# Performance work log

Measured on AMD Instinct MI355X. Metric: run time of the kernel, lower is better.

## Reference

```python
import jax, jax.numpy as jnp
import numpy as np
from jax import lax

EPS_GN = 1e-5
EPS_LN = 1e-5
EPS_ADJ = 1e-6


def group_norm(x, g, b, groups=8, eps=EPS_GN):
    # x: (N, C, T); PyTorch GroupNorm: normalize over (C//groups, T) per group
    N, C, T = x.shape
    xr = x.reshape(N, groups, C // groups, T)
    m = xr.mean(axis=(2, 3), keepdims=True)
    v = xr.var(axis=(2, 3), keepdims=True)
    xr = (xr - m) * lax.rsqrt(v + eps)
    return xr.reshape(N, C, T) * g[None, :, None] + b[None, :, None]


def layer_norm(x, g, b, eps=EPS_LN):
    m = x.mean(axis=-1, keepdims=True)
    v = x.var(axis=-1, keepdims=True)
    return (x - m) * lax.rsqrt(v + eps) * g + b


def conv1d(x, w, stride, pad):
    # x: (N, Cin, T), w: (Cout, Cin, K), no bias
    return lax.conv_general_dilated(x, w, window_strides=(stride,), padding=[(pad, pad)],
                                    dimension_numbers=('NCH', 'OIH', 'NCH'))


def setup_inputs() -> dict:
    key = jax.random.key(0)
    ks = jax.random.split(key, 16)
    B, C, T = 256, 4, 4096
    TW, D, N = 64, 128, 4
    x = jax.random.normal(ks[0], (B, C, T), dtype=jnp.float32)
    conv1_w = jax.random.normal(ks[1], (TW, 1, 9), dtype=jnp.float32) * 0.1
    gn1_g = jnp.ones((TW,), jnp.float32)
    gn1_b = jnp.zeros((TW,), jnp.float32)
    conv2_w = jax.random.normal(ks[2], (TW, TW, 7), dtype=jnp.float32) * 0.05
    gn2_g = jnp.ones((TW,), jnp.float32)
    gn2_b = jnp.zeros((TW,), jnp.float32)
    proj_w = jax.random.normal(ks[3], (D, TW), dtype=jnp.float32) * 0.1
    proj_b = jnp.zeros((D,), jnp.float32)
    A = jnp.eye(N, dtype=jnp.float32) + 0.05 * jax.random.normal(ks[4], (N, N), dtype=jnp.float32)
    lin1_w = jax.random.normal(ks[5], (D, D), dtype=jnp.float32) * 0.08
    ln1_g = jnp.ones((D,), jnp.float32)
    ln1_b = jnp.zeros((D,), jnp.float32)
    lin2_w = jax.random.normal(ks[6], (D, D), dtype=jnp.float32) * 0.08
    ln2_g = jnp.ones((D,), jnp.float32)
    ln2_b = jnp.zeros((D,), jnp.float32)
    on_g = jnp.ones((D,), jnp.float32)
    on_b = jnp.zeros((D,), jnp.float32)
    return dict(x=x, conv1_w=conv1_w, gn1_g=gn1_g, gn1_b=gn1_b, conv2_w=conv2_w,
                gn2_g=gn2_g, gn2_b=gn2_b, proj_w=proj_w, proj_b=proj_b, A=A,
                lin1_w=lin1_w, ln1_g=ln1_g, ln1_b=ln1_b, lin2_w=lin2_w,
                ln2_g=ln2_g, ln2_b=ln2_b, on_g=on_g, on_b=on_b)


def reference(x, conv1_w, gn1_g, gn1_b, conv2_w, gn2_g, gn2_b, proj_w, proj_b, A,
              lin1_w, ln1_g, ln1_b, lin2_w, ln2_g, ln2_b, on_g, on_b):
    B, C, T = x.shape
    D = proj_w.shape[0]
    # The per-channel Python loop in the original shares the same temporal net;
    # fold channels into the batch dim and run the convs once.
    h = x.reshape(B * C, 1, T)
    h = jax.nn.gelu(group_norm(conv1d(h, conv1_w, 2, 4), gn1_g, gn1_b), approximate=False)
    h = jax.nn.gelu(group_norm(conv1d(h, conv2_w, 2, 3), gn2_g, gn2_b), approximate=False)
    h = h.mean(axis=-1)                      # (B*C, TW)
    v = h @ proj_w.T + proj_b                # (B*C, D)
    H = v.reshape(B, C, D)                   # node features, N = C channels
    # normalized adjacency: D^{-1/2} (A + I) D^{-1/2}
    A_tilde = A + jnp.eye(A.shape[0], dtype=A.dtype)
    deg = A_tilde.sum(axis=1)
    d_inv_sqrt = (deg + EPS_ADJ) ** -0.5
    A_hat = d_inv_sqrt[:, None] * A_tilde * d_inv_sqrt[None, :]
    for lw, lg, lb in ((lin1_w, ln1_g, ln1_b), (lin2_w, ln2_g, ln2_b)):
        Hm = jnp.einsum('nm,bmd->bnd', A_hat, H)
        H = jax.nn.gelu(layer_norm(Hm @ lw.T, lg, lb), approximate=False)
    H = layer_norm(H, on_g, on_b)
    return H.mean(axis=1)                    # (B, D)
```

## Files before the change

kernel.cpp:

```cpp
#include <hip/hip_runtime.h>
#include <hip/hip_fp16.h>
#include <math.h>

#define NS   1024
#define TIN  4096
#define T1   2048
#define T2   1024
#define TW   64
#define NG   8
#define DD   128

typedef __attribute__((ext_vector_type(8))) _Float16 f16x8;
typedef __attribute__((ext_vector_type(4))) float    f32x4;

__device__ __forceinline__ float gelu_fast(float x) {
  float t = x * x;
  float p = fmaf(0.044715f, t, 1.0f);
  float u = 2.3022038f * x * p;
  float e = exp2f(u);
  float r = __builtin_amdgcn_rcpf(e + 1.0f);
  return fmaf(-x, r, x);
}

__global__ __launch_bounds__(64) void k_stats1(
    const float* __restrict__ x, const float* __restrict__ w1,
    float* __restrict__ stats1) {
  int n = blockIdx.x;
  __shared__ float xw[4112];
  const float* xr = x + (size_t)n * TIN;
  for (int i = threadIdx.x; i < 4112; i += 64) {
    int xi = i - 4;
    xw[i] = (xi >= 0 && xi < TIN) ? xr[xi] : 0.f;
  }
  __syncthreads();
  float C[45], S[9];
#pragma unroll
  for (int c = 0; c < 45; c++) C[c] = 0.f;
#pragma unroll
  for (int i = 0; i < 9; i++) S[i] = 0.f;
  int l = threadIdx.x;
  for (int j = 0; j < 32; j++) {
    int t = l + 64 * j;
    float w[9];
#pragma unroll
    for (int i = 0; i < 9; i++) w[i] = xw[2 * t + i];
#pragma unroll
    for (int i = 0; i < 9; i++) S[i] += w[i];
    int c = 0;
#pragma unroll
    for (int i = 0; i < 9; i++)
#pragma unroll
      for (int jj = i; jj < 9; jj++) { C[c] = fmaf(w[i], w[jj], C[c]); c++; }
  }
#pragma unroll
  for (int off = 1; off < 64; off <<= 1) {
#pragma unroll
    for (int i = 0; i < 9; i++) S[i] += __shfl_xor(S[i], off, 64);
#pragma unroll
    for (int c = 0; c < 45; c++) C[c] += __shfl_xor(C[c], off, 64);
  }
  float wv[9];
#pragma unroll
  for (int i = 0; i < 9; i++) wv[i] = w1[l * 9 + i];
  float sm = 0.f, sq = 0.f;
  {
    int c = 0;
#pragma unroll
    for (int i = 0; i < 9; i++) {
      sm = fmaf(wv[i], S[i], sm);
#pragma unroll
      for (int jj = i; jj < 9; jj++) {
        float f = (jj == i) ? wv[i] * wv[jj] : 2.f * wv[i] * wv[jj];
        sq = fmaf(f, C[c], sq); c++;
      }
    }
  }
#pragma unroll
  for (int off = 1; off < 8; off <<= 1) {
    sm += __shfl_xor(sm, off, 64);
    sq += __shfl_xor(sq, off, 64);
  }
  if ((l & 7) == 0) {
    float m = sm * (1.f / 16384.f);
    float v = sq * (1.f / 16384.f) - m * m;
    stats1[(n * NG + (l >> 3)) * 2 + 0] = m;
    stats1[(n * NG + (l >> 3)) * 2 + 1] = rsqrtf(v + 1e-5f);
  }
}

__global__ __launch_bounds__(256) void k_prep(
    const float* __restrict__ w2, const float* __restrict__ w1,
    _Float16* __restrict__ w2tf, _Float16* __restrict__ w1h) {
  int idx = blockIdx.x * 256 + threadIdx.x;
  if (idx < 7 * 64 * 64) {
    int kk = idx >> 12;
    int r = idx & 4095;
    int co = r >> 6, ci = r & 63;
    w2tf[idx] = (_Float16)w2[(co * 64 + ci) * 7 + kk];
  } else {
    int r = idx - 28672;
    if (r < 64 * 32) {
      int ci = r >> 5, k = r & 31;
      w1h[r] = (k < 9) ? (_Float16)w1[ci * 9 + k] : (_Float16)0.f;
    }
  }
}

__global__ __launch_bounds__(256, 6) void k_conv(
    const float* __restrict__ x, const _Float16* __restrict__ w1h,
    const float* __restrict__ g1, const float* __restrict__ b1,
    const float* __restrict__ stats1, const _Float16* __restrict__ w2tf,
    __half* __restrict__ y2, float* __restrict__ stats2) {
  constexpr int ROWS = 144, HS = 72;
  __shared__ _Float16 h1s[ROWS * HS];
  __shared__ _Float16 xh[320];
  __shared__ float scs[TW], bss[TW];

  const int tid = threadIdx.x;
  const int n = blockIdx.x >> 4;
  const int tile = blockIdx.x & 15;
  const int t0 = tile << 6;
  const bool chk = (tile == 0) || (tile == 15);

  const float* xr = x + (size_t)n * TIN;
  for (int i = tid; i < 320; i += 256) {
    int xi = 4 * t0 - 10 + i;
    xh[i] = (i < 278 && xi >= 0 && xi < TIN) ? (_Float16)xr[xi] : (_Float16)0.f;
  }
  if (tid < TW) {
    int ci = tid, g = ci >> 3;
    float m = stats1[(n * NG + g) * 2 + 0];
    float is = stats1[(n * NG + g) * 2 + 1];
    float s = is * g1[ci];
    scs[ci] = s;
    bss[ci] = b1[ci] - m * s;
  }
  __syncthreads();

  const int lane = tid & 63;
  const int wv = tid >> 6;
  const int m = lane & 15;
  const int q = lane >> 4;

  {
    f16x8 w1f[4];
#pragma unroll
    for (int nt = 0; nt < 4; nt++)
      w1f[nt] = *(const f16x8*)&w1h[(nt * 16 + m) * 32 + 8 * q];
    float sc4[4], bs4[4];
#pragma unroll
    for (int nt = 0; nt < 4; nt++) {
      sc4[nt] = scs[nt * 16 + m];
      bs4[nt] = bss[nt * 16 + m];
    }
    for (int mt = wv; mt < 9; mt += 4) {
      int r0 = mt * 16;
      int xi0 = 2 * (r0 + m) + 8 * q;
      uint4 uu;
      uu.x = *(const unsigned*)&xh[xi0 + 0];
      uu.y = *(const unsigned*)&xh[xi0 + 2];
      uu.z = *(const unsigned*)&xh[xi0 + 4];
      uu.w = *(const unsigned*)&xh[xi0 + 6];
      f16x8 af = __builtin_bit_cast(f16x8, uu);
      int rowb = r0 + 4 * q;
#pragma unroll
      for (int nt = 0; nt < 4; nt++) {
        f32x4 d = __builtin_amdgcn_mfma_f32_16x16x32_f16(
            af, w1f[nt], (f32x4){0.f, 0.f, 0.f, 0.f}, 0, 0, 0);
#pragma unroll
        for (int r = 0; r < 4; r++) {
          float v = gelu_fast(fmaf(d[r], sc4[nt], bs4[nt]));
          if (chk) {
            int tp = 2 * t0 - 3 + rowb + r;
            if ((unsigned)tp >= (unsigned)T1) v = 0.f;
          }
          h1s[(rowb + r) * HS + nt * 16 + m] = (_Float16)v;
        }
      }
    }
  }
  __syncthreads();

  const int co0 = wv * 16 + m;
  f32x4 acc[4];
#pragma unroll
  for (int mt = 0; mt < 4; mt++) acc[mt] = (f32x4){0.f, 0.f, 0.f, 0.f};

  for (int kk = 0; kk < 7; kk++) {
    f16x8 bfr[2];
#pragma unroll
    for (int ks = 0; ks < 2; ks++)
      bfr[ks] = *(const f16x8*)&w2tf[(kk * 64 + co0) * 64 + 32 * ks + 8 * q];
#pragma unroll
    for (int mt = 0; mt < 4; mt++) {
      int tl = 2 * (mt * 16 + m) + kk;
      f16x8 a0 = *(const f16x8*)&h1s[tl * HS + 8 * q];
      f16x8 a1 = *(const f16x8*)&h1s[tl * HS + 32 + 8 * q];
      acc[mt] = __builtin_amdgcn_mfma_f32_16x16x32_f16(a0, bfr[0], acc[mt], 0, 0, 0);
      acc[mt] = __builtin_amdgcn_mfma_f32_16x16x32_f16(a1, bfr[1], acc[mt], 0, 0, 0);
    }
  }

  float sum = 0.f, ssq = 0.f;
#pragma unroll
  for (int mt = 0; mt < 4; mt++)
#pragma unroll
    for (int r = 0; r < 4; r++) {
      float v = acc[mt][r];
      sum += v; ssq += v * v;
    }
  sum += __shfl_xor(sum, 1, 64);  ssq += __shfl_xor(ssq, 1, 64);
  sum += __shfl_xor(sum, 2, 64);  ssq += __shfl_xor(ssq, 2, 64);
  sum += __shfl_xor(sum, 4, 64);  ssq += __shfl_xor(ssq, 4, 64);
  sum += __shfl_xor(sum, 16, 64); ssq += __shfl_xor(ssq, 16, 64);
  sum += __shfl_xor(sum, 32, 64); ssq += __shfl_xor(ssq, 32, 64);
  if (lane == 0 || lane == 8) {
    int g = 2 * wv + (lane >> 3);
    atomicAdd(&stats2[(n * NG + g) * 2 + 0], sum);
    atomicAdd(&stats2[(n * NG + g) * 2 + 1], ssq);
  }

  __syncthreads();
  __half* tr = (__half*)h1s;
#pragma unroll
  for (int mt = 0; mt < 4; mt++)
#pragma unroll
    for (int r = 0; r < 4; r++) {
      int t = mt * 16 + q * 4 + r;
      tr[t * HS + co0] = __float2half(acc[mt][r]);
    }
  __syncthreads();
  for (int idx = tid; idx < 512; idx += 256) {
    int t = idx >> 3, c8 = (idx & 7) * 8;
    float4 v = *(float4*)&tr[t * HS + c8];
    *(float4*)&y2[((size_t)(n * 1024) + t0 + t) * 64 + c8] = v;
  }
}

__global__ __launch_bounds__(256) void k_gn2mean(
    const __half* __restrict__ y2, const float* __restrict__ stats2,
    const float* __restrict__ g2, const float* __restrict__ b2,
    float* __restrict__ hbar) {
  int n = blockIdx.x >> 2;
  int tq = blockIdx.x & 3;
  int coct = threadIdx.x & 7;
  int tsl = threadIdx.x >> 3;
  int co0 = coct * 8;
  float mn = stats2[(n * NG + coct) * 2 + 0] * (1.f / 8192.f);
  float e2 = stats2[(n * NG + coct) * 2 + 1] * (1.f / 8192.f);
  float istd = rsqrtf(e2 - mn * mn + 1e-5f);
  float sca[8], sh[8];
#pragma unroll
  for (int j = 0; j < 8; j++) {
    sca[j] = istd * g2[co0 + j];
    sh[j] = b2[co0 + j] - mn * sca[j];
  }
  const __half* base = y2 + (size_t)n * 65536 + tq * (256 * 64);
  float4 raw[8];
#pragma unroll
  for (int i = 0; i < 8; i++)
    raw[i] = *(const float4*)&base[(tsl + 32 * i) * 64 + co0];
  float a[8];
#pragma unroll
  for (int j = 0; j < 8; j++) a[j] = 0.f;
#pragma unroll
  for (int i = 0; i < 8; i++) {
    __half2 hh[4];
    *(float4*)hh = raw[i];
#pragma unroll
    for (int p = 0; p < 4; p++) {
      float2 f = __half22float2(hh[p]);
      a[2 * p]     += gelu_fast(fmaf(f.x, sca[2 * p], sh[2 * p]));
      a[2 * p + 1] += gelu_fast(fmaf(f.y, sca[2 * p + 1], sh[2 * p + 1]));
    }
  }
  __shared__ float red[32][64];
  *(float4*)&red[tsl][co0] = *(float4*)&a[0];
  *(float4*)&red[tsl][co0 + 4] = *(float4*)&a[4];
  __syncthreads();
  if (threadIdx.x < 64) {
    float s = 0.f;
#pragma unroll 8
    for (int r = 0; r < 32; r++) s += red[r][threadIdx.x];
    atomicAdd(&hbar[n * 64 + threadIdx.x], s);
  }
}

__global__ __launch_bounds__(256) void k_head(
    const float* __restrict__ hbar,
    const float* __restrict__ pw, const float* __restrict__ pb,
    const float* __restrict__ A,
    const float* __restrict__ l1w, const float* __restrict__ l1g, const float* __restrict__ l1b,
    const float* __restrict__ l2w, const float* __restrict__ l2g, const float* __restrict__ l2b,
    const float* __restrict__ og, const float* __restrict__ ob,
    float* __restrict__ out) {
  int b = blockIdx.x;
  __shared__ float h4[4][TW];
  __shared__ float H[4][DD];
  __shared__ float Hm[4][DD];
  __shared__ float Xs[4][DD];
  __shared__ float At[16], Ah[16], dinv[4];
  {
    int i = threadIdx.x;
    int c = i >> 6, k = i & 63;
    h4[c][k] = hbar[(b * 4 + c) * TW + k] * (1.f / 1024.f);
  }
  if (threadIdx.x < 16)
    At[threadIdx.x] = A[threadIdx.x] + ((threadIdx.x % 5) == 0 ? 1.f : 0.f);
  __syncthreads();
  if (threadIdx.x < 4) {
    float dg = At[threadIdx.x * 4] + At[threadIdx.x * 4 + 1] +
               At[threadIdx.x * 4 + 2] + At[threadIdx.x * 4 + 3];
    dinv[threadIdx.x] = rsqrtf(dg + 1e-6f);
  }
  for (int idx = threadIdx.x; idx < 512; idx += 256) {
    int c = idx >> 7, d = idx & 127;
    float acc = pb[d];
    const float* wrow = pw + d * TW;
#pragma unroll 8
    for (int k = 0; k < TW; k++) acc += h4[c][k] * wrow[k];
    H[c][d] = acc;
  }
  __syncthreads();
  if (threadIdx.x < 16)
    Ah[threadIdx.x] = dinv[threadIdx.x >> 2] * At[threadIdx.x] * dinv[threadIdx.x & 3];
  __syncthreads();
  for (int L = 0; L < 2; L++) {
    const float* lw = L ? l2w : l1w;
    const float* lg = L ? l2g : l1g;
    const float* lb = L ? l2b : l1b;
    for (int idx = threadIdx.x; idx < 512; idx += 256) {
      int nn = idx >> 7, d = idx & 127;
      Hm[nn][d] = Ah[nn * 4 + 0] * H[0][d] + Ah[nn * 4 + 1] * H[1][d] +
                  Ah[nn * 4 + 2] * H[2][d] + Ah[nn * 4 + 3] * H[3][d];
    }
    __syncthreads();
    for (int idx = threadIdx.x; idx < 512; idx += 256) {
      int nn = idx >> 7, d = idx & 127;
      float acc = 0.f;
      const float* wrow = lw + d * DD;
#pragma unroll 8
      for (int k = 0; k < DD; k++) acc += Hm[nn][k] * wrow[k];
      Xs[nn][d] = acc;
    }
    __syncthreads();
    {
      int w = threadIdx.x >> 6, lane = threadIdx.x & 63;
      float v0 = Xs[w][lane], v1 = Xs[w][lane + 64];
      float s = v0 + v1, qq = v0 * v0 + v1 * v1;
#pragma unroll
      for (int off = 1; off < 64; off <<= 1) {
        s += __shfl_xor(s, off, 64);
        qq += __shfl_xor(qq, off, 64);
      }
      float mm = s * (1.f / 128.f);
      float istd = rsqrtf(qq * (1.f / 128.f) - mm * mm + 1e-5f);
      H[w][lane]      = gelu_fast((v0 - mm) * istd * lg[lane] + lb[lane]);
      H[w][lane + 64] = gelu_fast((v1 - mm) * istd * lg[lane + 64] + lb[lane + 64]);
    }
    __syncthreads();
  }
  {
    int w = threadIdx.x >> 6, lane = threadIdx.x & 63;
    float v0 = H[w][lane], v1 = H[w][lane + 64];
    float s = v0 + v1, qq = v0 * v0 + v1 * v1;
#pragma unroll
    for (int off = 1; off < 64; off <<= 1) {
      s += __shfl_xor(s, off, 64);
      qq += __shfl_xor(qq, off, 64);
    }
    float mm = s * (1.f / 128.f);
    float istd = rsqrtf(qq * (1.f / 128.f) - mm * mm + 1e-5f);
    Xs[w][lane]      = (v0 - mm) * istd * og[lane] + ob[lane];
    Xs[w][lane + 64] = (v1 - mm) * istd * og[lane + 64] + ob[lane + 64];
  }
  __syncthreads();
  if (threadIdx.x < DD) {
    int d = threadIdx.x;
    out[b * DD + d] = 0.25f * (Xs[0][d] + Xs[1][d] + Xs[2][d] + Xs[3][d]);
  }
}

extern "C" void kernel_launch(void* const* d_in, const int* in_sizes, int n_in,
                              void* d_out, int out_size, void* d_ws, size_t ws_size,
                              hipStream_t stream) {
  (void)in_sizes; (void)n_in; (void)out_size; (void)ws_size;
  const float* x       = (const float*)d_in[0];
  const float* conv1_w = (const float*)d_in[1];
  const float* gn1_g   = (const float*)d_in[2];
  const float* gn1_b   = (const float*)d_in[3];
  const float* conv2_w = (const float*)d_in[4];
  const float* gn2_g   = (const float*)d_in[5];
  const float* gn2_b   = (const float*)d_in[6];
  const float* proj_w  = (const float*)d_in[7];
  const float* proj_b  = (const float*)d_in[8];
  const float* A       = (const float*)d_in[9];
  const float* lin1_w  = (const float*)d_in[10];
  const float* ln1_g   = (const float*)d_in[11];
  const float* ln1_b   = (const float*)d_in[12];
  const float* lin2_w  = (const float*)d_in[13];
  const float* ln2_g   = (const float*)d_in[14];
  const float* ln2_b   = (const float*)d_in[15];
  const float* on_g    = (const float*)d_in[16];
  const float* on_b    = (const float*)d_in[17];
  float* out = (float*)d_out;

  float* wsf = (float*)d_ws;
  float* stats2 = wsf;
  float* hbar   = wsf + 16384;
  float* stats1 = wsf + 81920;
  _Float16* w2tf = (_Float16*)(wsf + 98304);
  _Float16* w1h  = (_Float16*)(wsf + 112640);
  __half* y2h    = (__half*)(wsf + 113664);

  hipMemsetAsync(stats2, 0, (16384 + 65536) * sizeof(float), stream);
  k_prep<<<120, 256, 0, stream>>>(conv2_w, conv1_w, w2tf, w1h);
  k_stats1<<<NS, 64, 0, stream>>>(x, conv1_w, stats1);
  k_conv<<<NS * 16, 256, 0, stream>>>(x, w1h, gn1_g, gn1_b, stats1, w2tf,
                                      y2h, stats2);
  k_gn2mean<<<NS * 4, 256, 0, stream>>>(y2h, stats2, gn2_g, gn2_b, hbar);
  k_head<<<256, 256, 0, stream>>>(hbar, proj_w, proj_b, A,
                                  lin1_w, ln1_g, ln1_b,
                                  lin2_w, ln2_g, ln2_b,
                                  on_g, on_b, out);
}
```

Baseline: 326.0 us.

## Use 32x32x16 MFMA with larger conv tiles and fold weight prep into stats kernel

The conv kernel now processes 128 output timesteps per 512-thread block instead of 64 per 256-thread block. This shrinks the recomputed conv1 halo relative to the useful work. Both conv stages switch from 16x16x32 to 32x32x16 MFMA instructions, with a new w1 layout padded to 16 taps and rewritten stats reduction and output mapping. The separate weight-prep kernel is merged into the stats1 kernel as extra blocks, removing one launch. In exchange, LDS use per block doubles, which may lower occupancy, and the boundary check now runs on every tile.

```diff
diff --git a/kernel.cpp b/kernel.cpp
--- a/kernel.cpp
+++ b/kernel.cpp
@@ -10,8 +10,9 @@
 #define NG   8
 #define DD   128
 
-typedef __attribute__((ext_vector_type(8))) _Float16 f16x8;
-typedef __attribute__((ext_vector_type(4))) float    f32x4;
+typedef __attribute__((ext_vector_type(8)))  _Float16 f16x8;
+typedef __attribute__((ext_vector_type(4)))  float    f32x4;
+typedef __attribute__((ext_vector_type(16))) float    f32x16;
 
 __device__ __forceinline__ float gelu_fast(float x) {
   float t = x * x;
@@ -22,9 +23,27 @@
   return fmaf(-x, r, x);
 }
 
-__global__ __launch_bounds__(64) void k_stats1(
+__global__ __launch_bounds__(64) void k_prep_stats(
     const float* __restrict__ x, const float* __restrict__ w1,
-    float* __restrict__ stats1) {
+    const float* __restrict__ w2,
+    float* __restrict__ stats1, _Float16* __restrict__ w2tf,
+    _Float16* __restrict__ w1h16) {
+  if (blockIdx.x >= NS) {
+    int base = (blockIdx.x - NS) * 64 + threadIdx.x;
+    for (int i = base; i < 28672 + 1024; i += 128 * 64) {
+      if (i < 28672) {
+        int kk = i >> 12;
+        int r = i & 4095;
+        int co = r >> 6, ci = r & 63;
+        w2tf[i] = (_Float16)w2[(co * 64 + ci) * 7 + kk];
+      } else {
+        int r = i - 28672;
+        int co = r >> 4, k = r & 15;
+        w1h16[r] = (k < 9) ? (_Float16)w1[co * 9 + k] : (_Float16)0.f;
+      }
+    }
+    return;
+  }
   int n = blockIdx.x;
   __shared__ float xw[4112];
   const float* xr = x + (size_t)n * TIN;
@@ -88,44 +107,25 @@
   }
 }
 
-__global__ __launch_bounds__(256) void k_prep(
-    const float* __restrict__ w2, const float* __restrict__ w1,
-    _Float16* __restrict__ w2tf, _Float16* __restrict__ w1h) {
-  int idx = blockIdx.x * 256 + threadIdx.x;
-  if (idx < 7 * 64 * 64) {
-    int kk = idx >> 12;
-    int r = idx & 4095;
-    int co = r >> 6, ci = r & 63;
-    w2tf[idx] = (_Float16)w2[(co * 64 + ci) * 7 + kk];
-  } else {
-    int r = idx - 28672;
-    if (r < 64 * 32) {
-      int ci = r >> 5, k = r & 31;
-      w1h[r] = (k < 9) ? (_Float16)w1[ci * 9 + k] : (_Float16)0.f;
-    }
-  }
-}
-
-__global__ __launch_bounds__(256, 6) void k_conv(
-    const float* __restrict__ x, const _Float16* __restrict__ w1h,
+__global__ __launch_bounds__(512, 6) void k_conv(
+    const float* __restrict__ x, const _Float16* __restrict__ w1h16,
     const float* __restrict__ g1, const float* __restrict__ b1,
     const float* __restrict__ stats1, const _Float16* __restrict__ w2tf,
     __half* __restrict__ y2, float* __restrict__ stats2) {
-  constexpr int ROWS = 144, HS = 72;
+  constexpr int ROWS = 288, HS = 72;
   __shared__ _Float16 h1s[ROWS * HS];
-  __shared__ _Float16 xh[320];
+  __shared__ _Float16 xh[608];
   __shared__ float scs[TW], bss[TW];
 
   const int tid = threadIdx.x;
-  const int n = blockIdx.x >> 4;
-  const int tile = blockIdx.x & 15;
-  const int t0 = tile << 6;
-  const bool chk = (tile == 0) || (tile == 15);
+  const int n = blockIdx.x >> 3;
+  const int tile = blockIdx.x & 7;
+  const int t0 = tile << 7;
 
   const float* xr = x + (size_t)n * TIN;
-  for (int i = tid; i < 320; i += 256) {
+  for (int i = tid; i < 608; i += 512) {
     int xi = 4 * t0 - 10 + i;
-    xh[i] = (i < 278 && xi >= 0 && xi < TIN) ? (_Float16)xr[xi] : (_Float16)0.f;
+    xh[i] = (xi >= 0 && xi < TIN) ? (_Float16)xr[xi] : (_Float16)0.f;
   }
   if (tid < TW) {
     int ci = tid, g = ci >> 3;
@@ -139,83 +139,62 @@
 
   const int lane = tid & 63;
   const int wv = tid >> 6;
-  const int m = lane & 15;
-  const int q = lane >> 4;
-
-  {
-    f16x8 w1f[4];
-#pragma unroll
-    for (int nt = 0; nt < 4; nt++)
-      w1f[nt] = *(const f16x8*)&w1h[(nt * 16 + m) * 32 + 8 * q];
-    float sc4[4], bs4[4];
-#pragma unroll
-    for (int nt = 0; nt < 4; nt++) {
-      sc4[nt] = scs[nt * 16 + m];
-      bs4[nt] = bss[nt * 16 + m];
-    }
-    for (int mt = wv; mt < 9; mt += 4) {
-      int r0 = mt * 16;
-      int xi0 = 2 * (r0 + m) + 8 * q;
-      uint4 uu;
-      uu.x = *(const unsigned*)&xh[xi0 + 0];
-      uu.y = *(const unsigned*)&xh[xi0 + 2];
-      uu.z = *(const unsigned*)&xh[xi0 + 4];
-      uu.w = *(const unsigned*)&xh[xi0 + 6];
-      f16x8 af = __builtin_bit_cast(f16x8, uu);
-      int rowb = r0 + 4 * q;
-#pragma unroll
-      for (int nt = 0; nt < 4; nt++) {
-        f32x4 d = __builtin_amdgcn_mfma_f32_16x16x32_f16(
-            af, w1f[nt], (f32x4){0.f, 0.f, 0.f, 0.f}, 0, 0, 0);
-#pragma unroll
-        for (int r = 0; r < 4; r++) {
-          float v = gelu_fast(fmaf(d[r], sc4[nt], bs4[nt]));
-          if (chk) {
-            int tp = 2 * t0 - 3 + rowb + r;
-            if ((unsigned)tp >= (unsigned)T1) v = 0.f;
-          }
-          h1s[(rowb + r) * HS + nt * 16 + m] = (_Float16)v;
-        }
-      }
-    }
-  }
-  __syncthreads();
-
-  const int co0 = wv * 16 + m;
-  f32x4 acc[4];
-#pragma unroll
-  for (int mt = 0; mt < 4; mt++) acc[mt] = (f32x4){0.f, 0.f, 0.f, 0.f};
-
+  const int l31 = lane & 31;
+  const int l5 = lane >> 5;
+
+  for (int j = wv; j < 18; j += 8) {
+    int mtile = j >> 1, nt = j & 1;
+    int r0 = mtile * 32;
+    int xg = 2 * (r0 + l31) + 8 * l5;
+    uint4 uu;
+    uu.x = *(const unsigned*)&xh[xg + 0];
+    uu.y = *(const unsigned*)&xh[xg + 2];
+    uu.z = *(const unsigned*)&xh[xg + 4];
+    uu.w = *(const unsigned*)&xh[xg + 6];
+    f16x8 af = __builtin_bit_cast(f16x8, uu);
+    int coA = nt * 32 + l31;
+    f16x8 bf = *(const f16x8*)&w1h16[coA * 16 + 8 * l5];
+    f32x16 d = __builtin_amdgcn_mfma_f32_32x32x16_f16(
+        af, bf, (f32x16){0.f}, 0, 0, 0);
+    float sc = scs[coA], bs = bss[coA];
+#pragma unroll
+    for (int reg = 0; reg < 16; reg++) {
+      int row = r0 + (reg & 3) + 8 * (reg >> 2) + 4 * l5;
+      float v = gelu_fast(fmaf(d[reg], sc, bs));
+      int tp = 2 * t0 - 3 + row;
+      if ((unsigned)tp >= (unsigned)T1) v = 0.f;
+      h1s[row * HS + coA] = (_Float16)v;
+    }
+  }
+  __syncthreads();
+
+  const int tpart = wv & 3;
+  const int npart = wv >> 2;
+  const int co0 = npart * 32 + l31;
+  const int tl0 = 2 * (tpart * 32 + l31);
+  f32x16 acc = (f32x16){0.f};
+#pragma unroll
   for (int kk = 0; kk < 7; kk++) {
-    f16x8 bfr[2];
-#pragma unroll
-    for (int ks = 0; ks < 2; ks++)
-      bfr[ks] = *(const f16x8*)&w2tf[(kk * 64 + co0) * 64 + 32 * ks + 8 * q];
-#pragma unroll
-    for (int mt = 0; mt < 4; mt++) {
-      int tl = 2 * (mt * 16 + m) + kk;
-      f16x8 a0 = *(const f16x8*)&h1s[tl * HS + 8 * q];
-      f16x8 a1 = *(const f16x8*)&h1s[tl * HS + 32 + 8 * q];
-      acc[mt] = __builtin_amdgcn_mfma_f32_16x16x32_f16(a0, bfr[0], acc[mt], 0, 0, 0);
-      acc[mt] = __builtin_amdgcn_mfma_f32_16x16x32_f16(a1, bfr[1], acc[mt], 0, 0, 0);
+#pragma unroll
+    for (int c16 = 0; c16 < 4; c16++) {
+      f16x8 b = *(const f16x8*)&w2tf[(kk * 64 + co0) * 64 + c16 * 16 + 8 * l5];
+      f16x8 a = *(const f16x8*)&h1s[(tl0 + kk) * HS + c16 * 16 + 8 * l5];
+      acc = __builtin_amdgcn_mfma_f32_32x32x16_f16(a, b, acc, 0, 0, 0);
     }
   }
 
   float sum = 0.f, ssq = 0.f;
 #pragma unroll
-  for (int mt = 0; mt < 4; mt++)
-#pragma unroll
-    for (int r = 0; r < 4; r++) {
-      float v = acc[mt][r];
-      sum += v; ssq += v * v;
-    }
+  for (int reg = 0; reg < 16; reg++) {
+    float v = acc[reg];
+    sum += v; ssq += v * v;
+  }
+  sum += __shfl_xor(sum, 32, 64); ssq += __shfl_xor(ssq, 32, 64);
   sum += __shfl_xor(sum, 1, 64);  ssq += __shfl_xor(ssq, 1, 64);
   sum += __shfl_xor(sum, 2, 64);  ssq += __shfl_xor(ssq, 2, 64);
   sum += __shfl_xor(sum, 4, 64);  ssq += __shfl_xor(ssq, 4, 64);
-  sum += __shfl_xor(sum, 16, 64); ssq += __shfl_xor(ssq, 16, 64);
-  sum += __shfl_xor(sum, 32, 64); ssq += __shfl_xor(ssq, 32, 64);
-  if (lane == 0 || lane == 8) {
-    int g = 2 * wv + (lane >> 3);
+  if ((lane & 39) == 0) {
+    int g = npart * 4 + (lane >> 3);
     atomicAdd(&stats2[(n * NG + g) * 2 + 0], sum);
     atomicAdd(&stats2[(n * NG + g) * 2 + 1], ssq);
   }
@@ -223,14 +202,12 @@
   __syncthreads();
   __half* tr = (__half*)h1s;
 #pragma unroll
-  for (int mt = 0; mt < 4; mt++)
-#pragma unroll
-    for (int r = 0; r < 4; r++) {
-      int t = mt * 16 + q * 4 + r;
-      tr[t * HS + co0] = __float2half(acc[mt][r]);
-    }
-  __syncthreads();
-  for (int idx = tid; idx < 512; idx += 256) {
+  for (int reg = 0; reg < 16; reg++) {
+    int t = tpart * 32 + (reg & 3) + 8 * (reg >> 2) + 4 * l5;
+    tr[t * HS + co0] = __float2half(acc[reg]);
+  }
+  __syncthreads();
+  for (int idx = tid; idx < 1024; idx += 512) {
     int t = idx >> 3, c8 = (idx & 7) * 8;
     float4 v = *(float4*)&tr[t * HS + c8];
     *(float4*)&y2[((size_t)(n * 1024) + t0 + t) * 64 + c8] = v;
@@ -409,15 +386,15 @@
   float* stats2 = wsf;
   float* hbar   = wsf + 16384;
   float* stats1 = wsf + 81920;
-  _Float16* w2tf = (_Float16*)(wsf + 98304);
-  _Float16* w1h  = (_Float16*)(wsf + 112640);
-  __half* y2h    = (__half*)(wsf + 113664);
+  _Float16* w2tf  = (_Float16*)(wsf + 98304);
+  _Float16* w1h16 = (_Float16*)(wsf + 112640);
+  __half* y2h     = (__half*)(wsf + 113664);
 
   hipMemsetAsync(stats2, 0, (16384 + 65536) * sizeof(float), stream);
-  k_prep<<<120, 256, 0, stream>>>(conv2_w, conv1_w, w2tf, w1h);
-  k_stats1<<<NS, 64, 0, stream>>>(x, conv1_w, stats1);
-  k_conv<<<NS * 16, 256, 0, stream>>>(x, w1h, gn1_g, gn1_b, stats1, w2tf,
-                                      y2h, stats2);
+  k_prep_stats<<<NS + 128, 64, 0, stream>>>(x, conv1_w, conv2_w,
+                                            stats1, w2tf, w1h16);
+  k_conv<<<NS * 8, 512, 0, stream>>>(x, w1h16, gn1_g, gn1_b, stats1, w2tf,
+                                     y2h, stats2);
   k_gn2mean<<<NS * 4, 256, 0, stream>>>(y2h, stats2, gn2_g, gn2_b, hbar);
   k_head<<<256, 256, 0, stream>>>(hbar, proj_w, proj_b, A,
                                   lin1_w, ln1_g, ln1_b,
```

After: 400.8 us. 1.23x slower.

## Store conv2 intermediate as fp8, merge prep into stats kernel, raise occupancy

Applied to the files above, without the earlier changes.

The conv2 output buffer moves from fp16 to fp8 (packed conversion on store, packed fp8-to-f32 unpack in the GN2/mean kernel), which halves the bytes written and re-read for the largest intermediate. The weight-prep kernel is folded into the stats1 kernel as extra blocks to save a launch, and the conv kernel's launch bounds go from 6 to 7 blocks per SM. fp8 storage lowers the precision of pre-normalisation activations and could hurt accuracy, and the tighter occupancy hint may force register spills.

```diff
diff --git a/kernel.cpp b/kernel.cpp
--- a/kernel.cpp
+++ b/kernel.cpp
@@ -12,6 +12,7 @@
 
 typedef __attribute__((ext_vector_type(8))) _Float16 f16x8;
 typedef __attribute__((ext_vector_type(4))) float    f32x4;
+typedef __attribute__((ext_vector_type(2))) float    f32x2;
 
 __device__ __forceinline__ float gelu_fast(float x) {
   float t = x * x;
@@ -22,9 +23,27 @@
   return fmaf(-x, r, x);
 }
 
-__global__ __launch_bounds__(64) void k_stats1(
+__global__ __launch_bounds__(64) void k_prep_stats(
     const float* __restrict__ x, const float* __restrict__ w1,
-    float* __restrict__ stats1) {
+    const float* __restrict__ w2,
+    float* __restrict__ stats1, _Float16* __restrict__ w2tf,
+    _Float16* __restrict__ w1h) {
+  if (blockIdx.x >= NS) {
+    int base = (blockIdx.x - NS) * 64 + threadIdx.x;
+    for (int i = base; i < 28672 + 2048; i += 32 * 64) {
+      if (i < 28672) {
+        int kk = i >> 12;
+        int r = i & 4095;
+        int co = r >> 6, ci = r & 63;
+        w2tf[i] = (_Float16)w2[(co * 64 + ci) * 7 + kk];
+      } else {
+        int r = i - 28672;
+        int ci = r >> 5, k = r & 31;
+        w1h[r] = (k < 9) ? (_Float16)w1[ci * 9 + k] : (_Float16)0.f;
+      }
+    }
+    return;
+  }
   int n = blockIdx.x;
   __shared__ float xw[4112];
   const float* xr = x + (size_t)n * TIN;
@@ -88,31 +107,13 @@
   }
 }
 
-__global__ __launch_bounds__(256) void k_prep(
-    const float* __restrict__ w2, const float* __restrict__ w1,
-    _Float16* __restrict__ w2tf, _Float16* __restrict__ w1h) {
-  int idx = blockIdx.x * 256 + threadIdx.x;
-  if (idx < 7 * 64 * 64) {
-    int kk = idx >> 12;
-    int r = idx & 4095;
-    int co = r >> 6, ci = r & 63;
-    w2tf[idx] = (_Float16)w2[(co * 64 + ci) * 7 + kk];
-  } else {
-    int r = idx - 28672;
-    if (r < 64 * 32) {
-      int ci = r >> 5, k = r & 31;
-      w1h[r] = (k < 9) ? (_Float16)w1[ci * 9 + k] : (_Float16)0.f;
-    }
-  }
-}
-
-__global__ __launch_bounds__(256, 6) void k_conv(
+__global__ __launch_bounds__(256, 7) void k_conv(
     const float* __restrict__ x, const _Float16* __restrict__ w1h,
     const float* __restrict__ g1, const float* __restrict__ b1,
     const float* __restrict__ stats1, const _Float16* __restrict__ w2tf,
-    __half* __restrict__ y2, float* __restrict__ stats2) {
+    unsigned char* __restrict__ y2, float* __restrict__ stats2) {
   constexpr int ROWS = 144, HS = 72;
-  __shared__ _Float16 h1s[ROWS * HS];
+  __shared__ __align__(16) _Float16 h1s[ROWS * HS];
   __shared__ _Float16 xh[320];
   __shared__ float scs[TW], bss[TW];
 
@@ -221,24 +222,29 @@
   }
 
   __syncthreads();
-  __half* tr = (__half*)h1s;
-#pragma unroll
-  for (int mt = 0; mt < 4; mt++)
-#pragma unroll
-    for (int r = 0; r < 4; r++) {
-      int t = mt * 16 + q * 4 + r;
-      tr[t * HS + co0] = __float2half(acc[mt][r]);
-    }
-  __syncthreads();
-  for (int idx = tid; idx < 512; idx += 256) {
-    int t = idx >> 3, c8 = (idx & 7) * 8;
-    float4 v = *(float4*)&tr[t * HS + c8];
-    *(float4*)&y2[((size_t)(n * 1024) + t0 + t) * 64 + c8] = v;
+  unsigned char* tr8 = (unsigned char*)h1s;
+#pragma unroll
+  for (int mt = 0; mt < 4; mt++) {
+    unsigned p01 = (unsigned)__builtin_amdgcn_cvt_pk_fp8_f32(
+        acc[mt][0], acc[mt][1], 0, false);
+    unsigned p23 = (unsigned)__builtin_amdgcn_cvt_pk_fp8_f32(
+        acc[mt][2], acc[mt][3], 0, false);
+    int tb = mt * 16 + q * 4;
+    tr8[(tb + 0) * 80 + co0] = (unsigned char)(p01);
+    tr8[(tb + 1) * 80 + co0] = (unsigned char)(p01 >> 8);
+    tr8[(tb + 2) * 80 + co0] = (unsigned char)(p23);
+    tr8[(tb + 3) * 80 + co0] = (unsigned char)(p23 >> 8);
+  }
+  __syncthreads();
+  {
+    int t = tid >> 2, c16 = (tid & 3) * 16;
+    uint4 v = *(const uint4*)&tr8[t * 80 + c16];
+    *(uint4*)&y2[((size_t)(n * 1024) + t0 + t) * 64 + c16] = v;
   }
 }
 
 __global__ __launch_bounds__(256) void k_gn2mean(
-    const __half* __restrict__ y2, const float* __restrict__ stats2,
+    const unsigned char* __restrict__ y2, const float* __restrict__ stats2,
     const float* __restrict__ g2, const float* __restrict__ b2,
     float* __restrict__ hbar) {
   int n = blockIdx.x >> 2;
@@ -255,24 +261,28 @@
     sca[j] = istd * g2[co0 + j];
     sh[j] = b2[co0 + j] - mn * sca[j];
   }
-  const __half* base = y2 + (size_t)n * 65536 + tq * (256 * 64);
-  float4 raw[8];
+  const unsigned char* base = y2 + (size_t)n * 65536 + tq * (256 * 64);
+  uint2 raw[8];
 #pragma unroll
   for (int i = 0; i < 8; i++)
-    raw[i] = *(const float4*)&base[(tsl + 32 * i) * 64 + co0];
+    raw[i] = *(const uint2*)&base[(tsl + 32 * i) * 64 + co0];
   float a[8];
 #pragma unroll
   for (int j = 0; j < 8; j++) a[j] = 0.f;
 #pragma unroll
   for (int i = 0; i < 8; i++) {
-    __half2 hh[4];
-    *(float4*)hh = raw[i];
-#pragma unroll
-    for (int p = 0; p < 4; p++) {
-      float2 f = __half22float2(hh[p]);
-      a[2 * p]     += gelu_fast(fmaf(f.x, sca[2 * p], sh[2 * p]));
-      a[2 * p + 1] += gelu_fast(fmaf(f.y, sca[2 * p + 1], sh[2 * p + 1]));
-    }
+    f32x2 f0 = __builtin_amdgcn_cvt_pk_f32_fp8(raw[i].x, false);
+    f32x2 f1 = __builtin_amdgcn_cvt_pk_f32_fp8(raw[i].x, true);
+    f32x2 f2 = __builtin_amdgcn_cvt_pk_f32_fp8(raw[i].y, false);
+    f32x2 f3 = __builtin_amdgcn_cvt_pk_f32_fp8(raw[i].y, true);
+    a[0] += gelu_fast(fmaf(f0.x, sca[0], sh[0]));
+    a[1] += gelu_fast(fmaf(f0.y, sca[1], sh[1]));
+    a[2] += gelu_fast(fmaf(f1.x, sca[2], sh[2]));
+    a[3] += gelu_fast(fmaf(f1.y, sca[3], sh[3]));
+    a[4] += gelu_fast(fmaf(f2.x, sca[4], sh[4]));
+    a[5] += gelu_fast(fmaf(f2.y, sca[5], sh[5]));
+    a[6] += gelu_fast(fmaf(f3.x, sca[6], sh[6]));
+    a[7] += gelu_fast(fmaf(f3.y, sca[7], sh[7]));
   }
   __shared__ float red[32][64];
   *(float4*)&red[tsl][co0] = *(float4*)&a[0];
@@ -411,14 +421,14 @@
   float* stats1 = wsf + 81920;
   _Float16* w2tf = (_Float16*)(wsf + 98304);
   _Float16* w1h  = (_Float16*)(wsf + 112640);
-  __half* y2h    = (__half*)(wsf + 113664);
+  unsigned char* y2 = (unsigned char*)(wsf + 113664);
 
   hipMemsetAsync(stats2, 0, (16384 + 65536) * sizeof(float), stream);
-  k_prep<<<120, 256, 0, stream>>>(conv2_w, conv1_w, w2tf, w1h);
-  k_stats1<<<NS, 64, 0, stream>>>(x, conv1_w, stats1);
+  k_prep_stats<<<NS + 32, 64, 0, stream>>>(x, conv1_w, conv2_w,
+                                           stats1, w2tf, w1h);
   k_conv<<<NS * 16, 256, 0, stream>>>(x, w1h, gn1_g, gn1_b, stats1, w2tf,
-                                      y2h, stats2);
-  k_gn2mean<<<NS * 4, 256, 0, stream>>>(y2h, stats2, gn2_g, gn2_b, hbar);
+                                      y2, stats2);
+  k_gn2mean<<<NS * 4, 256, 0, stream>>>(y2, stats2, gn2_g, gn2_b, hbar);
   k_head<<<256, 256, 0, stream>>>(hbar, proj_w, proj_b, A,
                                   lin1_w, ln1_g, ln1_b,
                                   lin2_w, ln2_g, ln2_b,
```

New measurement: 311.7 us. 1.05x faster.
